# Kernel optimization log

Hardware: AMD Instinct MI355X
Metric: run time of the kernel (lower is better)

Reference implementation:

```python
import jax, jax.numpy as jnp
import numpy as np

N_SLOTS, KEY_DIM, VAL_DIM = 8192, 64, 64
B, S, TOPK = 8, 2048, 8


def setup_inputs() -> dict:
    key = jax.random.key(0)
    k1, k2, k3, k4, k5 = jax.random.split(key, 5)
    queries = jax.random.normal(k1, (B, S, KEY_DIM), dtype=jnp.float32)
    keys_mem = jax.random.normal(k2, (N_SLOTS, KEY_DIM), dtype=jnp.float32) * 0.02
    vals_mem = jax.random.normal(k3, (N_SLOTS, VAL_DIM), dtype=jnp.float32) * 0.02
    fast_vals = jax.random.normal(k4, (N_SLOTS, VAL_DIM), dtype=jnp.float32) * 0.01
    timestamps = jax.random.uniform(k5, (N_SLOTS,), dtype=jnp.float32)
    return {
        "queries": queries,
        "keys_mem": keys_mem,
        "vals_mem": vals_mem,
        "fast_vals": fast_vals,
        "timestamps": timestamps,
        "topk": TOPK,
    }


def reference(queries, keys_mem, vals_mem, fast_vals, timestamps, topk):
    # sim: [B, S, n_slots], scaled dot-product vs. memory keys
    scale = keys_mem.shape[1] ** (-0.5)
    sim = jnp.einsum("bsd,nd->bsn", queries, keys_mem) * scale
    # topk indices computed on detached scores (torch uses sim.detach())
    _, idx = jax.lax.top_k(jax.lax.stop_gradient(sim), topk)  # idx: [B, S, k]
    # gather topk similarities (torch does this via one-hot * sim; same math)
    sim_topk = jnp.take_along_axis(sim, idx, axis=-1)  # [B, S, k]
    # effective memory = slow + fast store; gather rows (torch: one_hot @ memory)
    effective_memory = vals_mem + fast_vals  # [n_slots, val_dim]
    gathered_vals = effective_memory[idx]  # [B, S, k, val_dim]
    attn_weights = jax.nn.softmax(sim_topk, axis=-1)  # [B, S, k]
    weighted_vals = gathered_vals * attn_weights[..., None]  # [B, S, k, val_dim]
    ts_retrieved = timestamps[idx]  # [B, S, k]
    return weighted_vals, idx, ts_retrieved
```

## Files before the change

kernel.cpp:

```cpp
#include <hip/hip_runtime.h>
#include <math.h>

#define NQ      16384
#define NSLOTS  8192
#define D       64
#define K       8

#define WV_ELEMS  (NQ * K * D)
#define IDX_OFF   (WV_ELEMS)
#define TSO_OFF   (IDX_OFF + NQ * K)

#define QPB_P   32
#define BLOCK_P 512
#define HALVES  2
#define SPW_P   (NSLOTS / HALVES / 8)
#define ITERS_P (SPW_P / 32)

#define QPB_R   16
#define BLOCK_R 256

#define POOL_SHORT_OFF 1572864
#define WS_NEED_NEW  (4u * 1024u * 1024u)
#define WS_NEED_OLD  (3u * 1024u * 1024u)

using short8   = __attribute__((ext_vector_type(8))) short;
using ushort8  = __attribute__((ext_vector_type(8))) unsigned short;
using bf16x8   = __attribute__((ext_vector_type(8))) __bf16;
using f32x4    = __attribute__((ext_vector_type(4))) float;

#define MFMA_BF16(A, B, C) __builtin_amdgcn_mfma_f32_16x16x32_bf16((A), (B), (C), 0, 0, 0)

__device__ __forceinline__ bf16x8 load_frag(const unsigned short* p) {
    short8 s = *reinterpret_cast<const short8*>(p);
    return __builtin_bit_cast(bf16x8, s);
}

__device__ __forceinline__ float packkey(float s, int code) {
    unsigned u = __float_as_uint(s) & 0xFFFFE000u;
    return __uint_as_float(u | (unsigned)code);
}

__device__ __forceinline__ void ins8(float (&tv)[8], float key) {
    float k2 = fmaxf(key, tv[0]);
    float o0 = fminf(tv[1], k2);
    float o1 = __builtin_amdgcn_fmed3f(tv[1], tv[2], k2);
    float o2 = __builtin_amdgcn_fmed3f(tv[2], tv[3], k2);
    float o3 = __builtin_amdgcn_fmed3f(tv[3], tv[4], k2);
    float o4 = __builtin_amdgcn_fmed3f(tv[4], tv[5], k2);
    float o5 = __builtin_amdgcn_fmed3f(tv[5], tv[6], k2);
    float o6 = __builtin_amdgcn_fmed3f(tv[6], tv[7], k2);
    float o7 = fmaxf(tv[7], k2);
    tv[0]=o0; tv[1]=o1; tv[2]=o2; tv[3]=o3; tv[4]=o4; tv[5]=o5; tv[6]=o6; tv[7]=o7;
}

__device__ __forceinline__ void cs(float& a, float& b) {
    const float lo = fminf(a, b), hi = fmaxf(a, b);
    a = lo; b = hi;
}
__device__ __forceinline__ void sort_bitonic8(float (&v)[8]) {
    cs(v[0],v[4]); cs(v[1],v[5]); cs(v[2],v[6]); cs(v[3],v[7]);
    cs(v[0],v[2]); cs(v[1],v[3]); cs(v[4],v[6]); cs(v[5],v[7]);
    cs(v[0],v[1]); cs(v[2],v[3]); cs(v[4],v[5]); cs(v[6],v[7]);
}

__device__ __forceinline__ void csu(unsigned long long& a, unsigned long long& b) {
    const bool lt = a < b;
    const unsigned long long lo = lt ? a : b;
    const unsigned long long hi = lt ? b : a;
    a = lo; b = hi;
}
__device__ __forceinline__ void sort_bitonic8_u64(unsigned long long (&v)[8]) {
    csu(v[0],v[4]); csu(v[1],v[5]); csu(v[2],v[6]); csu(v[3],v[7]);
    csu(v[0],v[2]); csu(v[1],v[3]); csu(v[4],v[6]); csu(v[5],v[7]);
    csu(v[0],v[1]); csu(v[2],v[3]); csu(v[4],v[5]); csu(v[6],v[7]);
}
__device__ __forceinline__ void sort8_u64(unsigned long long (&v)[8]) {
    csu(v[0],v[1]); csu(v[2],v[3]); csu(v[4],v[5]); csu(v[6],v[7]);
    csu(v[0],v[2]); csu(v[1],v[3]); csu(v[4],v[6]); csu(v[5],v[7]);
    csu(v[1],v[2]); csu(v[5],v[6]);
    csu(v[0],v[4]); csu(v[1],v[5]); csu(v[2],v[6]); csu(v[3],v[7]);
    csu(v[2],v[4]); csu(v[3],v[5]);
    csu(v[1],v[2]); csu(v[3],v[4]); csu(v[5],v[6]);
}

__device__ __forceinline__ unsigned short f2bf(float f) {
    unsigned u = __float_as_uint(f);
    return (unsigned short)((u + 0x7FFFu + ((u >> 16) & 1u)) >> 16);
}

__global__ __launch_bounds__(256)
void conv_kernel(const float* __restrict__ q, const float* __restrict__ k,
                 unsigned short* __restrict__ ws) {
    const int t = blockIdx.x * blockDim.x + threadIdx.x;
    if (t < 262144) {
        float4 v = reinterpret_cast<const float4*>(q)[t];
        unsigned long long r =
              (unsigned long long)f2bf(v.x * 0.125f)
            | ((unsigned long long)f2bf(v.y * 0.125f) << 16)
            | ((unsigned long long)f2bf(v.z * 0.125f) << 32)
            | ((unsigned long long)f2bf(v.w * 0.125f) << 48);
        reinterpret_cast<unsigned long long*>(ws + 524288)[t] = r;
    } else if (t < 393216) {
        const int i = t - 262144;
        float4 v = reinterpret_cast<const float4*>(k)[i];
        unsigned long long r =
              (unsigned long long)f2bf(v.x)
            | ((unsigned long long)f2bf(v.y) << 16)
            | ((unsigned long long)f2bf(v.z) << 32)
            | ((unsigned long long)f2bf(v.w) << 48);
        reinterpret_cast<unsigned long long*>(ws)[i] = r;
    }
}

__global__ __launch_bounds__(BLOCK_P, 8)
void ltm_prefilter_kernel(const unsigned short* __restrict__ kb,
                          const unsigned short* __restrict__ qb,
                          unsigned short* __restrict__ poolu)
{
    __shared__ float candk[QPB_P][68];

    const int tid  = threadIdx.x;
    const int lane = tid & 63;
    const int w    = tid >> 6;
    const int row  = lane & 15;
    const int g    = lane >> 4;
    const int g4   = g * 4;
    const int koff = g * 8;
    const int bid  = blockIdx.x;
    const int qbase = (bid >> 1) * QPB_P;
    const int half  = bid & 1;

    const unsigned short* qpA = qb + (size_t)(qbase + row) * D + koff;
    const bf16x8 bA0 = load_frag(qpA);
    const bf16x8 bA1 = load_frag(qpA + 32);
    const bf16x8 bB0 = load_frag(qpA + 16 * D);
    const bf16x8 bB1 = load_frag(qpA + 16 * D + 32);

    float tvA[8], tvB[8];
    #pragma unroll
    for (int i = 0; i < 8; ++i) { tvA[i] = -INFINITY; tvB[i] = -INFINITY; }

    const int wbase = half * (NSLOTS / HALVES) + w * SPW_P;

    const unsigned short* kp0 = kb + (size_t)(wbase + row) * D + koff;
    bf16x8 a00 = load_frag(kp0);
    bf16x8 a01 = load_frag(kp0 + 32);
    bf16x8 a10 = load_frag(kp0 + 16 * D);
    bf16x8 a11 = load_frag(kp0 + 16 * D + 32);

    int codeA = 8191 - (wbase + g4);

    #pragma unroll 2
    for (int it = 0; it < ITERS_P; ++it) {
        const int snext = wbase + (it + 1) * 32;
        const unsigned short* np_ = kb + (size_t)(snext + row) * D + koff;
        bf16x8 n00 = load_frag(np_);
        bf16x8 n01 = load_frag(np_ + 32);
        bf16x8 n10 = load_frag(np_ + 16 * D);
        bf16x8 n11 = load_frag(np_ + 16 * D + 32);

        const f32x4 z = {0.f, 0.f, 0.f, 0.f};
        f32x4 c00 = MFMA_BF16(a00, bA0, z);  c00 = MFMA_BF16(a01, bA1, c00);
        f32x4 c01 = MFMA_BF16(a00, bB0, z);  c01 = MFMA_BF16(a01, bB1, c01);
        f32x4 c10 = MFMA_BF16(a10, bA0, z);  c10 = MFMA_BF16(a11, bA1, c10);
        f32x4 c11 = MFMA_BF16(a10, bB0, z);  c11 = MFMA_BF16(a11, bB1, c11);

        ins8(tvA, packkey(c00[0], codeA     ));
        ins8(tvA, packkey(c00[1], codeA -  1));
        ins8(tvA, packkey(c00[2], codeA -  2));
        ins8(tvA, packkey(c00[3], codeA -  3));
        ins8(tvA, packkey(c10[0], codeA - 16));
        ins8(tvA, packkey(c10[1], codeA - 17));
        ins8(tvA, packkey(c10[2], codeA - 18));
        ins8(tvA, packkey(c10[3], codeA - 19));
        ins8(tvB, packkey(c01[0], codeA     ));
        ins8(tvB, packkey(c01[1], codeA -  1));
        ins8(tvB, packkey(c01[2], codeA -  2));
        ins8(tvB, packkey(c01[3], codeA -  3));
        ins8(tvB, packkey(c11[0], codeA - 16));
        ins8(tvB, packkey(c11[1], codeA - 17));
        ins8(tvB, packkey(c11[2], codeA - 18));
        ins8(tvB, packkey(c11[3], codeA - 19));

        codeA -= 32;
        a00 = n00; a01 = n01; a10 = n10; a11 = n11;
    }

    {
        float sA[8], sB[8];
        #pragma unroll
        for (int j = 0; j < 8; ++j) {
            sA[j] = __shfl_xor(tvA[j], 32, 64);
            sB[j] = __shfl_xor(tvB[j], 32, 64);
        }
        float mA[8], mB[8];
        #pragma unroll
        for (int j = 0; j < 8; ++j) {
            mA[j] = fmaxf(tvA[j], sA[7 - j]);
            mB[j] = fmaxf(tvB[j], sB[7 - j]);
        }
        sort_bitonic8(mA);
        sort_bitonic8(mB);
        #pragma unroll
        for (int j = 0; j < 8; ++j) {
            sA[j] = __shfl_xor(mA[j], 16, 64);
            sB[j] = __shfl_xor(mB[j], 16, 64);
        }
        float fA[8], fB[8];
        #pragma unroll
        for (int j = 0; j < 8; ++j) {
            fA[j] = fmaxf(mA[j], sA[7 - j]);
            fB[j] = fmaxf(mB[j], sB[7 - j]);
        }
        sort_bitonic8(fA);
        sort_bitonic8(fB);
        if (g == 0) {
            #pragma unroll
            for (int j = 0; j < 8; ++j) {
                candk[row     ][w * 8 + j] = fA[j];
                candk[row + 16][w * 8 + j] = fB[j];
            }
        }
    }
    __syncthreads();

    if (tid < 256) {
        const int  ql = tid >> 3;
        const int  jj = tid & 7;
        const bool hi = (jj & 1) != 0;

        float v[8];
        #pragma unroll
        for (int i = 0; i < 8; ++i) v[i] = candk[ql][jj * 8 + i];

        {
            float sk[8], mk[8];
            #pragma unroll
            for (int i = 0; i < 8; ++i) sk[i] = __shfl_xor(v[i], 1, 64);
            #pragma unroll
            for (int i = 0; i < 8; ++i)
                mk[i] = hi ? fmaxf(v[i], sk[7 - i]) : fminf(v[i], sk[7 - i]);
            sort_bitonic8(mk);
            #pragma unroll
            for (int i = 0; i < 8; ++i) v[i] = mk[i];
        }
        #pragma unroll
        for (int rnd = 0; rnd < 2; ++rnd) {
            const int st = rnd ? 5 : 3;
            float sk[8], mk[8], sk2[8];
            #pragma unroll
            for (int i = 0; i < 8; ++i) sk[i] = __shfl_xor(v[i], st, 64);
            #pragma unroll
            for (int i = 0; i < 8; ++i) mk[i] = fmaxf(v[i], sk[7 - i]);
            #pragma unroll
            for (int i = 0; i < 8; ++i) sk2[i] = __shfl_xor(mk[i], 1, 64);
            #pragma unroll
            for (int i = 0; i < 8; ++i)
                mk[i] = hi ? fmaxf(mk[i], sk2[i]) : fminf(mk[i], sk2[i]);
            sort_bitonic8(mk);
            #pragma unroll
            for (int i = 0; i < 8; ++i) v[i] = mk[i];
        }
        if (jj < 2) {
            ushort8 o;
            #pragma unroll
            for (int i = 0; i < 8; ++i)
                o[i] = (unsigned short)(8191u - (__float_as_uint(v[i]) & 8191u));
            *reinterpret_cast<ushort8*>(
                poolu + ((size_t)(qbase + ql) * 32 + half * 16 + jj * 8)) = o;
        }
    }
}

__global__ __launch_bounds__(BLOCK_R, 4)
void ltm_rescore_kernel(const float* __restrict__ queries,
                        const float* __restrict__ keys_mem,
                        const float* __restrict__ vals_mem,
                        const float* __restrict__ fast_vals,
                        const float* __restrict__ timestamps,
                        const unsigned short* __restrict__ poolu,
                        float* __restrict__ out)
{
    const int tid = threadIdx.x;
    const int ql  = tid >> 4;
    const int l16 = tid & 15;
    const int sg  = l16 >> 2;
    const int ls4 = l16 & 3;
    const int q   = blockIdx.x * QPB_R + ql;

    float4 qv4[4];
    {
        const float4* qp = reinterpret_cast<const float4*>(queries) + (size_t)q * 16 + ls4 * 4;
        #pragma unroll
        for (int i = 0; i < 4; ++i) qv4[i] = qp[i];
    }

    unsigned long long tk[8];
    #pragma unroll
    for (int jt = 0; jt < 8; ++jt) {
        const int sid = poolu[(size_t)q * 32 + sg * 8 + jt];
        const float4* kp = reinterpret_cast<const float4*>(keys_mem) + (size_t)sid * 16 + ls4 * 4;
        float p = 0.f;
        #pragma unroll
        for (int i = 0; i < 4; ++i) {
            const float4 kc = kp[i];
            p = fmaf(qv4[i].x, kc.x, p);
            p = fmaf(qv4[i].y, kc.y, p);
            p = fmaf(qv4[i].z, kc.z, p);
            p = fmaf(qv4[i].w, kc.w, p);
        }
        p += __shfl_xor(p, 1, 64);
        p += __shfl_xor(p, 2, 64);
        const float s = p * 0.125f;
        const unsigned u  = __float_as_uint(s);
        const unsigned ou = (u & 0x80000000u) ? ~u : (u | 0x80000000u);
        tk[jt] = ((unsigned long long)ou << 13) | (unsigned)(8191 - sid);
    }
    sort8_u64(tk);

    #pragma unroll
    for (int st = 4; st <= 8; st <<= 1) {
        unsigned long long sk[8], mk[8];
        #pragma unroll
        for (int j = 0; j < 8; ++j) sk[j] = __shfl_xor(tk[j], st, 64);
        #pragma unroll
        for (int j = 0; j < 8; ++j) {
            const unsigned long long a = tk[j], b = sk[7 - j];
            mk[j] = a > b ? a : b;
        }
        sort_bitonic8_u64(mk);
        #pragma unroll
        for (int j = 0; j < 8; ++j) tk[j] = mk[j];
    }

    float wv[K]; int wi[K];
    #pragma unroll
    for (int r = 0; r < K; ++r) {
        const unsigned long long best = tk[7 - r];
        const int      sid = 8191 - (int)(best & 8191ull);
        const unsigned ou  = (unsigned)(best >> 13);
        const unsigned ub  = (ou & 0x80000000u) ? (ou & 0x7FFFFFFFu) : ~ou;
        wv[r] = __uint_as_float(ub);
        wi[r] = sid;
    }
    const float m = wv[0];
    float e[K]; float sum = 0.f;
    #pragma unroll
    for (int r = 0; r < K; ++r) { e[r] = expf(wv[r] - m); sum += e[r]; }
    const float inv = 1.f / sum;

    {
        const int   r   = l16 >> 1;
        const int   h   = l16 & 1;
        const int   id  = wi[r];
        const float wgt = e[r] * inv;
        const float4* vp = reinterpret_cast<const float4*>(vals_mem)  + (size_t)id * 16 + h * 8;
        const float4* fp = reinterpret_cast<const float4*>(fast_vals) + (size_t)id * 16 + h * 8;
        float4* op = reinterpret_cast<float4*>(out) + ((size_t)(q * K + r)) * 16 + h * 8;
        #pragma unroll
        for (int i = 0; i < 8; ++i) {
            const float4 a = vp[i];
            const float4 b = fp[i];
            float4 c;
            c.x = (a.x + b.x) * wgt;
            c.y = (a.y + b.y) * wgt;
            c.z = (a.z + b.z) * wgt;
            c.w = (a.w + b.w) * wgt;
            op[i] = c;
        }
        if (l16 < 8) {
            out[IDX_OFF + (size_t)q * K + l16] = (float)wi[l16];
        } else {
            const int r2 = l16 - 8;
            out[TSO_OFF + (size_t)q * K + r2] = timestamps[wi[r2]];
        }
    }
}

#define QPB    32
#define BLOCK  512
#define WAVES  8
#define SPW    (NSLOTS / WAVES)
#define ITERS  (SPW / 32)

__global__ __launch_bounds__(BLOCK, 4)
void ltm_mfma_kernel(const float* __restrict__ queries,
                     const float* __restrict__ keys_mem,
                     const float* __restrict__ vals_mem,
                     const float* __restrict__ fast_vals,
                     const float* __restrict__ timestamps,
                     const unsigned short* __restrict__ kb,
                     const unsigned short* __restrict__ qb,
                     float* __restrict__ out)
{
    __shared__ float candk[QPB][68];

    const int tid  = threadIdx.x;
    const int lane = tid & 63;
    const int w    = tid >> 6;
    const int row  = lane & 15;
    const int g    = lane >> 4;
    const int g4   = g * 4;
    const int koff = g * 8;
    const int qbase = blockIdx.x * QPB;

    const unsigned short* qpA = qb + (size_t)(qbase + row) * D + koff;
    const bf16x8 bA0 = load_frag(qpA);
    const bf16x8 bA1 = load_frag(qpA + 32);
    const bf16x8 bB0 = load_frag(qpA + 16 * D);
    const bf16x8 bB1 = load_frag(qpA + 16 * D + 32);

    float tvA[8], tvB[8];
    #pragma unroll
    for (int i = 0; i < 8; ++i) { tvA[i] = -INFINITY; tvB[i] = -INFINITY; }

    const int wbase = w * SPW;
    const unsigned short* kp0 = kb + (size_t)(wbase + row) * D + koff;
    bf16x8 a00 = load_frag(kp0);
    bf16x8 a01 = load_frag(kp0 + 32);
    bf16x8 a10 = load_frag(kp0 + 16 * D);
    bf16x8 a11 = load_frag(kp0 + 16 * D + 32);

    int codeA = 8191 - (wbase + g4);

    #pragma unroll 2
    for (int it = 0; it < ITERS; ++it) {
        const int snext = wbase + (it + 1) * 32;
        const unsigned short* np_ = kb + (size_t)(snext + row) * D + koff;
        bf16x8 n00 = load_frag(np_);
        bf16x8 n01 = load_frag(np_ + 32);
        bf16x8 n10 = load_frag(np_ + 16 * D);
        bf16x8 n11 = load_frag(np_ + 16 * D + 32);

        const f32x4 z = {0.f, 0.f, 0.f, 0.f};
        f32x4 c00 = MFMA_BF16(a00, bA0, z);  c00 = MFMA_BF16(a01, bA1, c00);
        f32x4 c01 = MFMA_BF16(a00, bB0, z);  c01 = MFMA_BF16(a01, bB1, c01);
        f32x4 c10 = MFMA_BF16(a10, bA0, z);  c10 = MFMA_BF16(a11, bA1, c10);
        f32x4 c11 = MFMA_BF16(a10, bB0, z);  c11 = MFMA_BF16(a11, bB1, c11);

        ins8(tvA, packkey(c00[0], codeA     ));
        ins8(tvA, packkey(c00[1], codeA -  1));
        ins8(tvA, packkey(c00[2], codeA -  2));
        ins8(tvA, packkey(c00[3], codeA -  3));
        ins8(tvA, packkey(c10[0], codeA - 16));
        ins8(tvA, packkey(c10[1], codeA - 17));
        ins8(tvA, packkey(c10[2], codeA - 18));
        ins8(tvA, packkey(c10[3], codeA - 19));
        ins8(tvB, packkey(c01[0], codeA     ));
        ins8(tvB, packkey(c01[1], codeA -  1));
        ins8(tvB, packkey(c01[2], codeA -  2));
        ins8(tvB, packkey(c01[3], codeA -  3));
        ins8(tvB, packkey(c11[0], codeA - 16));
        ins8(tvB, packkey(c11[1], codeA - 17));
        ins8(tvB, packkey(c11[2], codeA - 18));
        ins8(tvB, packkey(c11[3], codeA - 19));

        codeA -= 32;
        a00 = n00; a01 = n01; a10 = n10; a11 = n11;
    }

    {
        float sA[8], sB[8];
        #pragma unroll
        for (int j = 0; j < 8; ++j) {
            sA[j] = __shfl_xor(tvA[j], 32, 64);
            sB[j] = __shfl_xor(tvB[j], 32, 64);
        }
        float mA[8], mB[8];
        #pragma unroll
        for (int j = 0; j < 8; ++j) {
            mA[j] = fmaxf(tvA[j], sA[7 - j]);
            mB[j] = fmaxf(tvB[j], sB[7 - j]);
        }
        sort_bitonic8(mA);
        sort_bitonic8(mB);
        #pragma unroll
        for (int j = 0; j < 8; ++j) {
            sA[j] = __shfl_xor(mA[j], 16, 64);
            sB[j] = __shfl_xor(mB[j], 16, 64);
        }
        if (g == 0) {
            #pragma unroll
            for (int j = 0; j < 8; ++j) {
                candk[row     ][w * 8 + j] = fmaxf(mA[j], sA[7 - j]);
                candk[row + 16][w * 8 + j] = fmaxf(mB[j], sB[7 - j]);
            }
        }
    }
    __syncthreads();

    const int ql  = tid >> 4;
    const int l16 = tid & 15;
    const int sg  = l16 >> 2;
    const int ls4 = l16 & 3;
    const int q   = qbase + ql;

    float4 qv4[4];
    {
        const float4* qp = reinterpret_cast<const float4*>(queries) + (size_t)q * 16 + ls4 * 4;
        #pragma unroll
        for (int i = 0; i < 4; ++i) qv4[i] = qp[i];
    }

    unsigned long long tk[8];
    #pragma unroll
    for (int i = 0; i < 8; ++i) tk[i] = 0ull;

    #pragma unroll 4
    for (int jt = 0; jt < 16; ++jt) {
        const float fk  = candk[ql][sg * 16 + jt];
        const int   sid = 8191 - (int)(__float_as_uint(fk) & 8191u);
        const float4* kp = reinterpret_cast<const float4*>(keys_mem) + (size_t)sid * 16 + ls4 * 4;
        float p = 0.f;
        #pragma unroll
        for (int i = 0; i < 4; ++i) {
            const float4 kc = kp[i];
            p = fmaf(qv4[i].x, kc.x, p);
            p = fmaf(qv4[i].y, kc.y, p);
            p = fmaf(qv4[i].z, kc.z, p);
            p = fmaf(qv4[i].w, kc.w, p);
        }
        p += __shfl_xor(p, 1, 64);
        p += __shfl_xor(p, 2, 64);
        const float s = p * 0.125f;
        const unsigned u  = __float_as_uint(s);
        const unsigned ou = (u & 0x80000000u) ? ~u : (u | 0x80000000u);
        const unsigned long long key =
            ((unsigned long long)ou << 13) | (unsigned)(8191 - sid);
        if (key > tk[0]) {
            tk[0] = key;
            #pragma unroll
            for (int uu = 0; uu < 7; ++uu) {
                const bool sw = tk[uu] > tk[uu + 1];
                const unsigned long long x = sw ? tk[uu + 1] : tk[uu];
                const unsigned long long y = sw ? tk[uu]     : tk[uu + 1];
                tk[uu] = x; tk[uu + 1] = y;
            }
        }
    }

    #pragma unroll
    for (int st = 4; st <= 8; st <<= 1) {
        unsigned long long sk[8], mk[8];
        #pragma unroll
        for (int j = 0; j < 8; ++j) sk[j] = __shfl_xor(tk[j], st, 64);
        #pragma unroll
        for (int j = 0; j < 8; ++j) {
            const unsigned long long a = tk[j], b = sk[7 - j];
            mk[j] = a > b ? a : b;
        }
        sort_bitonic8_u64(mk);
        #pragma unroll
        for (int j = 0; j < 8; ++j) tk[j] = mk[j];
    }

    float wv[K]; int wi[K];
    #pragma unroll
    for (int r = 0; r < K; ++r) {
        const unsigned long long best = tk[7 - r];
        const int      sid = 8191 - (int)(best & 8191ull);
        const unsigned ou  = (unsigned)(best >> 13);
        const unsigned ub  = (ou & 0x80000000u) ? (ou & 0x7FFFFFFFu) : ~ou;
        wv[r] = __uint_as_float(ub);
        wi[r] = sid;
    }
    const float m = wv[0];
    float e[K]; float sum = 0.f;
    #pragma unroll
    for (int r = 0; r < K; ++r) { e[r] = expf(wv[r] - m); sum += e[r]; }
    const float inv = 1.f / sum;

    {
        const int   r   = l16 >> 1;
        const int   h   = l16 & 1;
        const int   id  = wi[r];
        const float wgt = e[r] * inv;
        const float4* vp = reinterpret_cast<const float4*>(vals_mem)  + (size_t)id * 16 + h * 8;
        const float4* fp = reinterpret_cast<const float4*>(fast_vals) + (size_t)id * 16 + h * 8;
        float4* op = reinterpret_cast<float4*>(out) + ((size_t)(q * K + r)) * 16 + h * 8;
        #pragma unroll
        for (int i = 0; i < 8; ++i) {
            const float4 a = vp[i];
            const float4 b = fp[i];
            float4 c;
            c.x = (a.x + b.x) * wgt;
            c.y = (a.y + b.y) * wgt;
            c.z = (a.z + b.z) * wgt;
            c.w = (a.w + b.w) * wgt;
            op[i] = c;
        }
        if (l16 < 8) {
            out[IDX_OFF + (size_t)q * K + l16] = (float)wi[l16];
        } else {
            const int r2 = l16 - 8;
            out[TSO_OFF + (size_t)q * K + r2] = timestamps[wi[r2]];
        }
    }
}

#define FQPB   32
#define FTPQ   8
#define FBLOCK 256
#define FTS    128
#define FLDK   68
#define FNTILES (NSLOTS / FTS)

__global__ __launch_bounds__(FBLOCK, 2)
void ltm_fused_kernel(const float* __restrict__ queries,
                      const float* __restrict__ keys_mem,
                      const float* __restrict__ vals_mem,
                      const float* __restrict__ fast_vals,
                      const float* __restrict__ timestamps,
                      float* __restrict__ out)
{
    __shared__ float kt[FTS * FLDK];
    __shared__ float candv[FQPB][FTPQ * K];
    __shared__ int   candi[FQPB][FTPQ * K];
    __shared__ float selw[FQPB][K];
    __shared__ int   seli[FQPB][K];

    const int tid = threadIdx.x;
    const int ql  = tid / FTPQ;
    const int sub = tid % FTPQ;
    const int q   = blockIdx.x * FQPB + ql;

    float4 qv[D / 4];
    {
        const float4* qp = reinterpret_cast<const float4*>(queries + (size_t)q * D);
        #pragma unroll
        for (int i = 0; i < D / 4; ++i) qv[i] = qp[i];
    }

    float tv[K]; int ti[K];
    #pragma unroll
    for (int i = 0; i < K; ++i) { tv[i] = -INFINITY; ti[i] = 0; }

    for (int tile = 0; tile < FNTILES; ++tile) {
        __syncthreads();
        {
            const float4* kg = reinterpret_cast<const float4*>(keys_mem + (size_t)tile * FTS * D);
            #pragma unroll
            for (int i = 0; i < (FTS * D / 4) / FBLOCK; ++i) {
                const int e = tid + i * FBLOCK;
                const int row = e >> 4;
                const int col = e & 15;
                *reinterpret_cast<float4*>(&kt[row * FLDK + col * 4]) = kg[e];
            }
        }
        __syncthreads();

        #pragma unroll 4
        for (int j = 0; j < FTS / FTPQ; ++j) {
            const int local = sub + j * FTPQ;
            const float* kr = &kt[local * FLDK];
            float4 a0 = make_float4(0.f, 0.f, 0.f, 0.f);
            float4 a1 = make_float4(0.f, 0.f, 0.f, 0.f);
            #pragma unroll
            for (int i = 0; i < D / 4; i += 2) {
                const float4 k0 = *reinterpret_cast<const float4*>(&kr[(i + 0) * 4]);
                const float4 k1 = *reinterpret_cast<const float4*>(&kr[(i + 1) * 4]);
                a0.x = fmaf(k0.x, qv[i].x, a0.x);   a0.y = fmaf(k0.y, qv[i].y, a0.y);
                a0.z = fmaf(k0.z, qv[i].z, a0.z);   a0.w = fmaf(k0.w, qv[i].w, a0.w);
                a1.x = fmaf(k1.x, qv[i+1].x, a1.x); a1.y = fmaf(k1.y, qv[i+1].y, a1.y);
                a1.z = fmaf(k1.z, qv[i+1].z, a1.z); a1.w = fmaf(k1.w, qv[i+1].w, a1.w);
            }
            float s = ((a0.x + a1.x) + (a0.y + a1.y)) + ((a0.z + a1.z) + (a0.w + a1.w));
            s *= 0.125f;
            const int gid = tile * FTS + local;
            if (s > tv[0]) {
                tv[0] = s; ti[0] = gid;
                #pragma unroll
                for (int u = 0; u < K - 1; ++u) {
                    const bool sw = tv[u] > tv[u + 1];
                    const float va = sw ? tv[u + 1] : tv[u];
                    const float vb = sw ? tv[u]     : tv[u + 1];
                    const int   ia = sw ? ti[u + 1] : ti[u];
                    const int   ib = sw ? ti[u]     : ti[u + 1];
                    tv[u] = va; tv[u + 1] = vb; ti[u] = ia; ti[u + 1] = ib;
                }
            }
        }
    }

    #pragma unroll
    for (int i = 0; i < K; ++i) {
        candv[ql][sub * K + i] = tv[i];
        candi[ql][sub * K + i] = ti[i];
    }
    __syncthreads();

    if (sub == 0) {
        float wv[K]; int wi[K];
        #pragma unroll
        for (int r = 0; r < K; ++r) {
            float bv = -INFINITY; int bi = 0x7fffffff; int bp = 0;
            for (int c = 0; c < FTPQ * K; ++c) {
                const float v = candv[ql][c];
                const int  id = candi[ql][c];
                if ((v > bv) || (v == bv && id < bi)) { bv = v; bi = id; bp = c; }
            }
            candv[ql][bp] = -INFINITY;
            wv[r] = bv; wi[r] = bi;
        }
        const float m = wv[0];
        float e[K]; float sum = 0.f;
        #pragma unroll
        for (int r = 0; r < K; ++r) { e[r] = expf(wv[r] - m); sum += e[r]; }
        const float inv = 1.f / sum;
        #pragma unroll
        for (int r = 0; r < K; ++r) { selw[ql][r] = e[r] * inv; seli[ql][r] = wi[r]; }
    }
    __syncthreads();

    {
        const int r = sub;
        const int id = seli[ql][r];
        const float w = selw[ql][r];
        const float4* vp = reinterpret_cast<const float4*>(vals_mem  + (size_t)id * D);
        const float4* fp = reinterpret_cast<const float4*>(fast_vals + (size_t)id * D);
        float4* op = reinterpret_cast<float4*>(out + (size_t)(q * K + r) * D);
        #pragma unroll
        for (int i = 0; i < D / 4; ++i) {
            const float4 a = vp[i];
            const float4 b = fp[i];
            float4 c;
            c.x = (a.x + b.x) * w; c.y = (a.y + b.y) * w;
            c.z = (a.z + b.z) * w; c.w = (a.w + b.w) * w;
            op[i] = c;
        }
        out[IDX_OFF + (size_t)q * K + r] = (float)id;
        out[TSO_OFF + (size_t)q * K + r] = timestamps[id];
    }
}

extern "C" void kernel_launch(void* const* d_in, const int* in_sizes, int n_in,
                              void* d_out, int out_size, void* d_ws, size_t ws_size,
                              hipStream_t stream) {
    (void)in_sizes; (void)n_in; (void)out_size;
    const float* queries    = (const float*)d_in[0];
    const float* keys_mem   = (const float*)d_in[1];
    const float* vals_mem   = (const float*)d_in[2];
    const float* fast_vals  = (const float*)d_in[3];
    const float* timestamps = (const float*)d_in[4];
    float* out = (float*)d_out;

    if (ws_size >= WS_NEED_NEW) {
        unsigned short* ws = (unsigned short*)d_ws;
        unsigned short* poolu = ws + POOL_SHORT_OFF;
        conv_kernel<<<1536, 256, 0, stream>>>(queries, keys_mem, ws);
        ltm_prefilter_kernel<<<(NQ / QPB_P) * HALVES, BLOCK_P, 0, stream>>>(
            ws , ws + 524288 , poolu);
        ltm_rescore_kernel<<<NQ / QPB_R, BLOCK_R, 0, stream>>>(
            queries, keys_mem, vals_mem, fast_vals, timestamps, poolu, out);
    } else if (ws_size >= WS_NEED_OLD) {
        unsigned short* ws = (unsigned short*)d_ws;
        conv_kernel<<<1536, 256, 0, stream>>>(queries, keys_mem, ws);
        ltm_mfma_kernel<<<NQ / QPB, BLOCK, 0, stream>>>(
            queries, keys_mem, vals_mem, fast_vals, timestamps,
            ws , ws + 524288 , out);
    } else {
        ltm_fused_kernel<<<NQ / FQPB, FBLOCK, 0, stream>>>(
            queries, keys_mem, vals_mem, fast_vals, timestamps, out);
    }
}
```

Measured before the change: 112.2 us.

## Use 32 threads per query in rescore kernel to halve per-thread work

The rescore kernel now assigns 32 lanes per query instead of 16, with 8 queries per 256-thread block. Each lane scores 4 candidates instead of 8, sorts them with a small 4-element network padded to 8, and joins one extra shuffle-merge stage. The weighted-value write is spread over 4 lanes per row. Launch bounds now target 8 blocks per SM. The aim is more parallelism and lower per-thread latency in the rescoring phase, at the cost of an extra cross-lane merge round and more blocks.

```diff
diff --git a/kernel.cpp b/kernel.cpp
--- a/kernel.cpp
+++ b/kernel.cpp
@@ -16,7 +16,7 @@
 #define SPW_P   (NSLOTS / HALVES / 8)
 #define ITERS_P (SPW_P / 32)
 
-#define QPB_R   16
+#define QPB_R   8
 #define BLOCK_R 256
 
 #define POOL_SHORT_OFF 1572864
@@ -73,14 +73,6 @@
     csu(v[0],v[4]); csu(v[1],v[5]); csu(v[2],v[6]); csu(v[3],v[7]);
     csu(v[0],v[2]); csu(v[1],v[3]); csu(v[4],v[6]); csu(v[5],v[7]);
     csu(v[0],v[1]); csu(v[2],v[3]); csu(v[4],v[5]); csu(v[6],v[7]);
-}
-__device__ __forceinline__ void sort8_u64(unsigned long long (&v)[8]) {
-    csu(v[0],v[1]); csu(v[2],v[3]); csu(v[4],v[5]); csu(v[6],v[7]);
-    csu(v[0],v[2]); csu(v[1],v[3]); csu(v[4],v[6]); csu(v[5],v[7]);
-    csu(v[1],v[2]); csu(v[5],v[6]);
-    csu(v[0],v[4]); csu(v[1],v[5]); csu(v[2],v[6]); csu(v[3],v[7]);
-    csu(v[2],v[4]); csu(v[3],v[5]);
-    csu(v[1],v[2]); csu(v[3],v[4]); csu(v[5],v[6]);
 }
 
 __device__ __forceinline__ unsigned short f2bf(float f) {
@@ -272,7 +264,7 @@
     }
 }
 
-__global__ __launch_bounds__(BLOCK_R, 4)
+__global__ __launch_bounds__(BLOCK_R, 8)
 void ltm_rescore_kernel(const float* __restrict__ queries,
                         const float* __restrict__ keys_mem,
                         const float* __restrict__ vals_mem,
@@ -282,10 +274,10 @@
                         float* __restrict__ out)
 {
     const int tid = threadIdx.x;
-    const int ql  = tid >> 4;
-    const int l16 = tid & 15;
-    const int sg  = l16 >> 2;
-    const int ls4 = l16 & 3;
+    const int ql  = tid >> 5;
+    const int l32 = tid & 31;
+    const int sg  = l32 >> 2;
+    const int ls4 = l32 & 3;
     const int q   = blockIdx.x * QPB_R + ql;
 
     float4 qv4[4];
@@ -295,10 +287,10 @@
         for (int i = 0; i < 4; ++i) qv4[i] = qp[i];
     }
 
-    unsigned long long tk[8];
-    #pragma unroll
-    for (int jt = 0; jt < 8; ++jt) {
-        const int sid = poolu[(size_t)q * 32 + sg * 8 + jt];
+    unsigned long long kk[4];
+    #pragma unroll
+    for (int jt = 0; jt < 4; ++jt) {
+        const int sid = poolu[(size_t)q * 32 + sg * 4 + jt];
         const float4* kp = reinterpret_cast<const float4*>(keys_mem) + (size_t)sid * 16 + ls4 * 4;
         float p = 0.f;
         #pragma unroll
@@ -314,12 +306,17 @@
         const float s = p * 0.125f;
         const unsigned u  = __float_as_uint(s);
         const unsigned ou = (u & 0x80000000u) ? ~u : (u | 0x80000000u);
-        tk[jt] = ((unsigned long long)ou << 13) | (unsigned)(8191 - sid);
-    }
-    sort8_u64(tk);
-
-    #pragma unroll
-    for (int st = 4; st <= 8; st <<= 1) {
+        kk[jt] = ((unsigned long long)ou << 13) | (unsigned)(8191 - sid);
+    }
+    csu(kk[0], kk[1]); csu(kk[2], kk[3]);
+    csu(kk[0], kk[2]); csu(kk[1], kk[3]);
+    csu(kk[1], kk[2]);
+    unsigned long long tk[8];
+    tk[0] = 0ull; tk[1] = 0ull; tk[2] = 0ull; tk[3] = 0ull;
+    tk[4] = kk[0]; tk[5] = kk[1]; tk[6] = kk[2]; tk[7] = kk[3];
+
+    #pragma unroll
+    for (int st = 4; st <= 16; st <<= 1) {
         unsigned long long sk[8], mk[8];
         #pragma unroll
         for (int j = 0; j < 8; ++j) sk[j] = __shfl_xor(tk[j], st, 64);
@@ -350,15 +347,15 @@
     const float inv = 1.f / sum;
 
     {
-        const int   r   = l16 >> 1;
-        const int   h   = l16 & 1;
+        const int   r   = l32 >> 2;
+        const int   s4  = l32 & 3;
         const int   id  = wi[r];
         const float wgt = e[r] * inv;
-        const float4* vp = reinterpret_cast<const float4*>(vals_mem)  + (size_t)id * 16 + h * 8;
-        const float4* fp = reinterpret_cast<const float4*>(fast_vals) + (size_t)id * 16 + h * 8;
-        float4* op = reinterpret_cast<float4*>(out) + ((size_t)(q * K + r)) * 16 + h * 8;
-        #pragma unroll
-        for (int i = 0; i < 8; ++i) {
+        const float4* vp = reinterpret_cast<const float4*>(vals_mem)  + (size_t)id * 16 + s4 * 4;
+        const float4* fp = reinterpret_cast<const float4*>(fast_vals) + (size_t)id * 16 + s4 * 4;
+        float4* op = reinterpret_cast<float4*>(out) + ((size_t)(q * K + r)) * 16 + s4 * 4;
+        #pragma unroll
+        for (int i = 0; i < 4; ++i) {
             const float4 a = vp[i];
             const float4 b = fp[i];
             float4 c;
@@ -368,10 +365,10 @@
             c.w = (a.w + b.w) * wgt;
             op[i] = c;
         }
-        if (l16 < 8) {
-            out[IDX_OFF + (size_t)q * K + l16] = (float)wi[l16];
-        } else {
-            const int r2 = l16 - 8;
+        if (l32 < 8) {
+            out[IDX_OFF + (size_t)q * K + l32] = (float)wi[l32];
+        } else if (l32 < 16) {
+            const int r2 = l32 - 8;
             out[TSO_OFF + (size_t)q * K + r2] = timestamps[wi[r2]];
         }
     }
```

Result: faster. 107.0 us, median of 2 (-4.6%).
